# Performance work log

Hardware: AMD Instinct MI355X
Metric: run time of the kernel (lower is better)

The kernel has to match this reference:

```python
import jax, jax.numpy as jnp
import numpy as np

B, F, L, P, H = 32, 64, 8192, 96, 8
HD = F // H
EPS_ATTN = 1e-6
EPS_REVIN = 1e-5
EPS_LN = 1e-5


def setup_inputs() -> dict:
    key = jax.random.key(0)
    ks = jax.random.split(key, 8)
    f32 = jnp.float32
    return {
        'x': jax.random.normal(ks[0], (B, F, L), dtype=f32),
        'gamma': jnp.ones((1, 1, F), dtype=f32),
        'beta': jnp.zeros((1, 1, F), dtype=f32),
        'ln_w': jnp.ones((F,), dtype=f32),
        'ln_b': jnp.zeros((F,), dtype=f32),
        'Wq': 0.05 * jax.random.normal(ks[1], (F, F), dtype=f32),
        'bq': jnp.zeros((F,), dtype=f32),
        'Wk': 0.05 * jax.random.normal(ks[2], (F, F), dtype=f32),
        'bk': jnp.zeros((F,), dtype=f32),
        'Wv': 0.05 * jax.random.normal(ks[3], (F, F), dtype=f32),
        'bv': jnp.zeros((F,), dtype=f32),
        'Wo': 0.05 * jax.random.normal(ks[4], (F, F), dtype=f32),
        'bo': jnp.zeros((F,), dtype=f32),
        'Wlin': 0.01 * jax.random.normal(ks[5], (P, L), dtype=f32),
        'blin': jnp.zeros((P,), dtype=f32),
        'Wp': 0.1 * jax.random.normal(ks[6], (1, F), dtype=f32),
        'bp': jnp.zeros((1,), dtype=f32),
    }


def _phi(t):
    # feature map: elu(x) + 1 (non-negative)
    return jax.nn.elu(t) + 1.0


def _layernorm(h, w, b):
    mu = jnp.mean(h, axis=-1, keepdims=True)
    var = jnp.mean(jnp.square(h - mu), axis=-1, keepdims=True)
    return (h - mu) * jax.lax.rsqrt(var + EPS_LN) * w + b


def reference(x, gamma, beta, ln_w, ln_b, Wq, bq, Wk, bk, Wv, bv, Wo, bo,
              Wlin, blin, Wp, bp):
    # (B, F, L) -> (B, L, F)
    xt = jnp.transpose(x, (0, 2, 1))
    # RevIN norm (stats over time axis, detached; torch std is unbiased ddof=1)
    mean = jax.lax.stop_gradient(jnp.mean(xt, axis=1, keepdims=True))
    std = jax.lax.stop_gradient(jnp.std(xt, axis=1, keepdims=True, ddof=1) + EPS_REVIN)
    xn = (xt - mean) / std * gamma + beta
    residual = xn
    h = _layernorm(xn, ln_w, ln_b)
    # Q/K/V projections (torch Linear: h @ W.T + b)
    Q = h @ Wq.T + bq
    K = h @ Wk.T + bk
    V = h @ Wv.T + bv
    # (B, L, F) -> (B, H, L, HD)
    def heads(t):
        return jnp.transpose(t.reshape(B, L, H, HD), (0, 2, 1, 3))
    Q, K, V = heads(Q), heads(K), heads(V)
    Q, K = _phi(Q), _phi(K)
    # linear attention: phi(Q) (phi(K)^T V) / (phi(Q) sum_n phi(K))
    KV = jnp.einsum('bhnd,bhne->bhde', K, V)           # (B,H,HD,HD)
    out = jnp.einsum('bhnd,bhde->bhne', Q, KV)          # (B,H,L,HD)
    Z = jnp.sum(K, axis=2)                              # (B,H,HD)
    normalizer = jnp.einsum('bhnd,bhd->bhn', Q, Z)[..., None] + EPS_ATTN
    out = out / normalizer
    out = jnp.transpose(out, (0, 2, 1, 3)).reshape(B, L, F)
    out = out @ Wo.T + bo
    y = out + residual                                  # (B, L, F)
    # temporal linear: (B, F, L) @ Wlin.T -> (B, F, P) -> (B, P, F)
    y = jnp.transpose(jnp.transpose(y, (0, 2, 1)) @ Wlin.T + blin, (0, 2, 1))
    # RevIN denorm
    y = (y - beta) / gamma
    y = y * std + mean
    # projector to scalar per step
    return (y @ Wp.T + bp)[..., 0]                      # (B, P)
```

## Files before the change

kernel.cpp:

```cpp
#include <hip/hip_runtime.h>
#include <cstddef>

#define NB 32
#define NF 64
#define NL 8192
#define NP 96
#define NH 8
#define TSPLIT 32

#define WS_MEAN 0
#define WS_STD  2048
#define WS_RSTD 4096
#define WS_KV   6144
#define WS_Z    22528
#define WS_OUT2 24576
#define WS_MUN  221184
#define WS_RSN  483328
#define WS_WLB  745472
#define WS_XNB  1138688
#define WS_YT   9527296

typedef __bf16 bfx8 __attribute__((ext_vector_type(8)));
typedef float f32x4 __attribute__((ext_vector_type(4)));
#define MFMA16(a, b, c) __builtin_amdgcn_mfma_f32_16x16x32_bf16((a), (b), (c), 0, 0, 0)

__device__ __forceinline__ unsigned short f2bf(float f) {
  unsigned u = __float_as_uint(f);
  unsigned r = u + 0x7FFFu + ((u >> 16) & 1u);
  return (unsigned short)(r >> 16);
}
__device__ __forceinline__ unsigned packbf2(float lo, float hi) {
  return (unsigned)f2bf(lo) | ((unsigned)f2bf(hi) << 16);
}
__device__ __forceinline__ float bflo(unsigned d) { return __uint_as_float(d << 16); }
__device__ __forceinline__ float bfhi(unsigned d) { return __uint_as_float(d & 0xFFFF0000u); }
__device__ __forceinline__ float bf1(unsigned short s) { return __uint_as_float(((unsigned)s) << 16); }

__device__ __forceinline__ bfx8 ldfrag(const unsigned short* p) {
  uint4 u = *(const uint4*)p;
  return __builtin_bit_cast(bfx8, u);
}

__global__ __launch_bounds__(256) void k_pre(
    const float* __restrict__ x, const float* __restrict__ Wlin,
    float* __restrict__ wmean, float* __restrict__ wstd, float* __restrict__ wrstd,
    unsigned short* __restrict__ wlb, float* __restrict__ zz) {
  __shared__ float r1[4], r2[4];
  const int bid = blockIdx.x, tid = threadIdx.x;
  if (bid < NB * NF) {
    const float4* row4 = (const float4*)(x + (size_t)bid * NL);
    float s1 = 0.f, s2 = 0.f;
#pragma unroll
    for (int i = 0; i < NL / 4 / 256; i++) {
      float4 v = row4[tid + i * 256];
      s1 += v.x + v.y + v.z + v.w;
      s2 += v.x * v.x + v.y * v.y + v.z * v.z + v.w * v.w;
    }
#pragma unroll
    for (int off = 32; off > 0; off >>= 1) {
      s1 += __shfl_down(s1, off, 64);
      s2 += __shfl_down(s2, off, 64);
    }
    if ((tid & 63) == 0) { r1[tid >> 6] = s1; r2[tid >> 6] = s2; }
    __syncthreads();
    if (tid == 0) {
      s1 = r1[0] + r1[1] + r1[2] + r1[3];
      s2 = r2[0] + r2[1] + r2[2] + r2[3];
      float m = s1 * (1.f / NL);
      float var = (s2 - (float)NL * m * m) * (1.f / (NL - 1));
      float sd = sqrtf(fmaxf(var, 0.f)) + 1e-5f;
      wmean[bid] = m;
      wstd[bid] = sd;
      wrstd[bid] = 1.f / sd;
    }
    unsigned zi = (unsigned)bid * 256u + (unsigned)tid;
    if (zi < 215040u) zz[zi] = 0.f;
  } else {
    int i = (bid - NB * NF) * 256 + tid;
    int p = i >> 10;
    int l8 = (i & 1023) * 8;
    float4 va = *(const float4*)&Wlin[(size_t)p * NL + l8];
    float4 vb = *(const float4*)&Wlin[(size_t)p * NL + l8 + 4];
    uint4 o;
    o.x = packbf2(va.x, va.y); o.y = packbf2(va.z, va.w);
    o.z = packbf2(vb.x, vb.y); o.w = packbf2(vb.z, vb.w);
    *(uint4*)&wlb[(((size_t)(l8 >> 5)) * NP + p) * 32 + (l8 & 31)] = o;
  }
}

__global__ __launch_bounds__(256, 4) void k_kv(
    const float* __restrict__ x,
    const float* __restrict__ gamma, const float* __restrict__ beta,
    const float* __restrict__ lnw, const float* __restrict__ lnb,
    const float* __restrict__ Wk, const float* __restrict__ bk,
    const float* __restrict__ Wv, const float* __restrict__ bv,
    const float* __restrict__ wmean, const float* __restrict__ wrstd,
    float* __restrict__ wKV, float* __restrict__ wZ,
    float* __restrict__ wmun, float* __restrict__ wrsn,
    unsigned short* __restrict__ xnb) {
  __shared__ __align__(16) char smem[39936];
  unsigned short* hA  = (unsigned short*)smem;
  unsigned short* WkB = (unsigned short*)(smem + 18432);
  unsigned short* WvB = (unsigned short*)(smem + 27648);
  unsigned short* pK  = (unsigned short*)smem;
  unsigned short* pV  = (unsigned short*)(smem + 17408);
  float* SkT  = (float*)(smem + 36864);
  float* Tful = (float*)(smem + 37888);
  float* mun  = (float*)(smem + 38400);
  float* rsn  = (float*)(smem + 38912);
  float* cbc  = (float*)(smem + 39424);

  const int tid = threadIdx.x;
  const int b = blockIdx.x >> 6;
  const int tI = blockIdx.x & 63;
  const int L0 = tI * 128;
  const int lane = tid & 63, wv = tid >> 6;
  const int mm = lane & 15, qd = lane >> 4;

  if (tid < 64) {
    float cb = wrstd[b * NF + tid] * gamma[tid];
    cbc[2 * tid] = cb;
    cbc[2 * tid + 1] = beta[tid] - wmean[b * NF + tid] * cb;
  }
  {
    int jj = tid >> 2, g = tid & 3;
    int f0 = g * 16;
    float tkp = 0.f, tvp = 0.f;
#pragma unroll
    for (int i = 0; i < 4; i++) {
      int f = f0 + i * 4;
      float4 wk4 = *(const float4*)&Wk[jj * NF + f];
      float4 wv4 = *(const float4*)&Wv[jj * NF + f];
      float4 lw  = *(const float4*)&lnw[f];
      float4 lb  = *(const float4*)&lnb[f];
      uint2 pk2, pv2;
      pk2.x = packbf2(wk4.x * lw.x, wk4.y * lw.y);
      pk2.y = packbf2(wk4.z * lw.z, wk4.w * lw.w);
      pv2.x = packbf2(wv4.x * lw.x, wv4.y * lw.y);
      pv2.y = packbf2(wv4.z * lw.z, wv4.w * lw.w);
      *(uint2*)&WkB[jj * 72 + f] = pk2;
      *(uint2*)&WvB[jj * 72 + f] = pv2;
      tkp += lb.x * wk4.x + lb.y * wk4.y + lb.z * wk4.z + lb.w * wk4.w;
      tvp += lb.x * wv4.x + lb.y * wv4.y + lb.z * wv4.z + lb.w * wv4.w;
    }
    tkp += __shfl_xor(tkp, 1, 64); tkp += __shfl_xor(tkp, 2, 64);
    tvp += __shfl_xor(tvp, 1, 64); tvp += __shfl_xor(tvp, 2, 64);
    if (g == 0) { Tful[jj] = tkp; Tful[64 + jj] = tvp; }
  }
  __syncthreads();

  {
    const int l = tid >> 1, fh = tid & 1;
    const float* xp = x + ((size_t)(b * NF + fh * 32)) * NL + L0 + l;
    const float4* cb4 = (const float4*)&cbc[fh * 64];
    float s1 = 0.f, s2 = 0.f;
    unsigned pw[16];
#pragma unroll
    for (int f2 = 0; f2 < 16; f2++) {
      float4 c = cb4[f2];
      float v0 = xp[(size_t)(2 * f2) * NL];
      float v1 = xp[(size_t)(2 * f2 + 1) * NL];
      float a0 = fmaf(v0, c.x, c.y);
      float a1 = fmaf(v1, c.z, c.w);
      s1 += a0 + a1;
      s2 += fmaf(a0, a0, a1 * a1);
      pw[f2] = packbf2(a0, a1);
    }
    uint4 q[4];
#pragma unroll
    for (int i = 0; i < 4; i++) {
      q[i].x = pw[4 * i]; q[i].y = pw[4 * i + 1];
      q[i].z = pw[4 * i + 2]; q[i].w = pw[4 * i + 3];
    }
    uint4* hd = (uint4*)&hA[l * 72 + fh * 32];
    uint4* gd = (uint4*)(xnb + (((size_t)(b * 64 + tI) * 128 + l) * 64 + fh * 32));
#pragma unroll
    for (int i = 0; i < 4; i++) { hd[i] = q[i]; gd[i] = q[i]; }
    s1 += __shfl_xor(s1, 1, 64);
    s2 += __shfl_xor(s2, 1, 64);
    if (fh == 0) {
      float mu = s1 * (1.f / NF);
      float var = s2 * (1.f / NF) - mu * mu;
      float rs = rsqrtf(fmaxf(var, 0.f) + 1e-5f);
      mun[l] = mu; rsn[l] = rs;
      wmun[(size_t)b * NL + L0 + l] = mu;
      wrsn[(size_t)b * NL + L0 + l] = rs;
    }
  }
  if (tid >= 128) {
    int sel = (tid >> 6) - 2, j = tid & 63;
    const unsigned* wr = (const unsigned*)((sel ? WvB : WkB) + j * 72);
    float s = 0.f;
#pragma unroll
    for (int i = 0; i < 32; i++) { unsigned d = wr[i]; s += bflo(d) + bfhi(d); }
    float t = Tful[sel * 64 + j] + (sel ? bv[j] : bk[j]);
    SkT[sel * 128 + j] = s;
    SkT[sel * 128 + 64 + j] = t;
  }
  __syncthreads();

  const f32x4 fz = {0.f, 0.f, 0.f, 0.f};
  f32x4 kacc[2][4], vacc[2][4];
#pragma unroll
  for (int i = 0; i < 2; i++)
#pragma unroll
    for (int jt = 0; jt < 4; jt++) { kacc[i][jt] = fz; vacc[i][jt] = fz; }

#pragma unroll
  for (int kc = 0; kc < 2; kc++) {
    bfx8 a0 = ldfrag(&hA[(wv * 32 + mm) * 72 + kc * 32 + qd * 8]);
    bfx8 a1 = ldfrag(&hA[(wv * 32 + 16 + mm) * 72 + kc * 32 + qd * 8]);
#pragma unroll
    for (int jt = 0; jt < 4; jt++) {
      bfx8 bkf = ldfrag(&WkB[(jt * 16 + mm) * 72 + kc * 32 + qd * 8]);
      bfx8 bvf = ldfrag(&WvB[(jt * 16 + mm) * 72 + kc * 32 + qd * 8]);
      kacc[0][jt] = MFMA16(a0, bkf, kacc[0][jt]);
      kacc[1][jt] = MFMA16(a1, bkf, kacc[1][jt]);
      vacc[0][jt] = MFMA16(a0, bvf, vacc[0][jt]);
      vacc[1][jt] = MFMA16(a1, bvf, vacc[1][jt]);
    }
  }

#pragma unroll
  for (int lt2 = 0; lt2 < 2; lt2++) {
    float4 mu4 = *(const float4*)&mun[wv * 32 + lt2 * 16 + qd * 4];
    float4 rs4 = *(const float4*)&rsn[wv * 32 + lt2 * 16 + qd * 4];
    float muv[4] = {mu4.x, mu4.y, mu4.z, mu4.w};
    float rsv[4] = {rs4.x, rs4.y, rs4.z, rs4.w};
#pragma unroll
    for (int jt = 0; jt < 4; jt++) {
      int j = jt * 16 + mm;
      float Sk = SkT[j], Tk = SkT[64 + j], Sv = SkT[128 + j], Tv = SkT[192 + j];
#pragma unroll
      for (int r = 0; r < 4; r++) {
        float kk = rsv[r] * (kacc[lt2][jt][r] - muv[r] * Sk) + Tk;
        kacc[lt2][jt][r] = (kk > 0.f) ? (kk + 1.f) : __expf(kk);
        vacc[lt2][jt][r] = rsv[r] * (vacc[lt2][jt][r] - muv[r] * Sv) + Tv;
      }
    }
  }
  __syncthreads();

#pragma unroll
  for (int lt2 = 0; lt2 < 2; lt2++) {
    int l0 = wv * 32 + lt2 * 16 + qd * 4;
#pragma unroll
    for (int jt = 0; jt < 4; jt++) {
      int j = jt * 16 + mm;
      uint2 dk, dv;
      dk.x = packbf2(kacc[lt2][jt][0], kacc[lt2][jt][1]);
      dk.y = packbf2(kacc[lt2][jt][2], kacc[lt2][jt][3]);
      dv.x = packbf2(vacc[lt2][jt][0], vacc[lt2][jt][1]);
      dv.y = packbf2(vacc[lt2][jt][2], vacc[lt2][jt][3]);
      *(uint2*)&pK[j * 136 + l0] = dk;
      *(uint2*)&pV[j * 136 + l0] = dv;
    }
  }
  __syncthreads();

  {
    f32x4 racc = fz;
#pragma unroll
    for (int kb = 0; kb < 4; kb++) {
      bfx8 ak = ldfrag(&pK[(wv * 16 + mm) * 136 + kb * 32 + qd * 8]);
      bfx8 bv8 = ldfrag(&pV[(wv * 16 + mm) * 136 + kb * 32 + qd * 8]);
      racc = MFMA16(ak, bv8, racc);
    }
    int eh = mm >> 3, e = mm & 7;
#pragma unroll
    for (int r = 0; r < 4; r++) {
      int row = qd * 4 + r;
      if ((row >> 3) == eh)
        atomicAdd(&wKV[(b * NH + wv * 2 + eh) * 64 + (row & 7) * 8 + e], racc[r]);
    }
  }
  if (tid < 64) {
    const unsigned* kr = (const unsigned*)&pK[tid * 136];
    float zs = 0.f;
#pragma unroll
    for (int i = 0; i < 64; i++) { unsigned d = kr[i]; zs += bflo(d) + bfhi(d); }
    atomicAdd(&wZ[b * 64 + tid], zs);
  }
}

__global__ __launch_bounds__(256, 3) void k_qy(
    const unsigned short* __restrict__ xnb,
    const float* __restrict__ lnw, const float* __restrict__ lnb,
    const float* __restrict__ Wq, const float* __restrict__ bq,
    const float* __restrict__ Wo, const float* __restrict__ bo,
    const float* __restrict__ wmun, const float* __restrict__ wrsn,
    const float* __restrict__ wKV, const float* __restrict__ wZ,
    unsigned short* __restrict__ ytb) {
  __shared__ __align__(16) char smem[41728];
  unsigned short* hA  = (unsigned short*)smem;
  unsigned short* qaA = (unsigned short*)smem;
  unsigned short* WqB = (unsigned short*)(smem + 18432);
  unsigned short* WoB = (unsigned short*)(smem + 27648);
  float* kvz   = (float*)(smem + 36864);
  float* mun   = (float*)(smem + 39168);
  float* rsn   = (float*)(smem + 39680);
  float* SqTq  = (float*)(smem + 40192);
  float* Tpart = (float*)(smem + 40704);

  const int tid = threadIdx.x;
  const int b = blockIdx.x >> 6;
  const int tI = blockIdx.x & 63;
  const int L0 = tI * 128;
  const int lane = tid & 63, wv = tid >> 6;
  const int mm = lane & 15, qd = lane >> 4;
  const unsigned short* xtile = xnb + (size_t)(b * 64 + tI) * 128 * 64;

  {
    int jj = tid >> 2, g = tid & 3;
    int f0 = g * 16;
    float tqp = 0.f;
#pragma unroll
    for (int i = 0; i < 4; i++) {
      int f = f0 + i * 4;
      float4 wq4 = *(const float4*)&Wq[jj * NF + f];
      float4 wo4 = *(const float4*)&Wo[jj * NF + f];
      float4 lw  = *(const float4*)&lnw[f];
      float4 lb  = *(const float4*)&lnb[f];
      uint2 pq2, po2;
      pq2.x = packbf2(wq4.x * lw.x, wq4.y * lw.y);
      pq2.y = packbf2(wq4.z * lw.z, wq4.w * lw.w);
      po2.x = packbf2(wo4.x, wo4.y);
      po2.y = packbf2(wo4.z, wo4.w);
      *(uint2*)&WqB[jj * 72 + f] = pq2;
      *(uint2*)&WoB[jj * 72 + f] = po2;
      tqp += lb.x * wq4.x + lb.y * wq4.y + lb.z * wq4.z + lb.w * wq4.w;
    }
    Tpart[g * 64 + jj] = tqp;
  }
  for (int i = tid; i < 576; i += 256)
    kvz[i] = (i < 512) ? wKV[b * 512 + i] : wZ[b * 64 + i - 512];
  {
    int row = tid >> 1, half = tid & 1;
    const uint4* s4 = (const uint4*)(xtile + (size_t)row * 64 + half * 32);
    uint4 u0 = s4[0], u1 = s4[1], u2 = s4[2], u3 = s4[3];
    uint4* d4 = (uint4*)&hA[row * 72 + half * 32];
    d4[0] = u0; d4[1] = u1; d4[2] = u2; d4[3] = u3;
  }
  if (tid < 128) {
    mun[tid] = wmun[(size_t)b * NL + L0 + tid];
    rsn[tid] = wrsn[(size_t)b * NL + L0 + tid];
  }
  __syncthreads();

  if (tid < 64) {
    const unsigned* wr = (const unsigned*)(WqB + tid * 72);
    float s = 0.f;
#pragma unroll
    for (int i = 0; i < 32; i++) { unsigned d = wr[i]; s += bflo(d) + bfhi(d); }
    float t = Tpart[tid] + Tpart[64 + tid] + Tpart[128 + tid] + Tpart[192 + tid] + bq[tid];
    SqTq[tid] = s; SqTq[64 + tid] = t;
  }
  __syncthreads();

  const f32x4 fz = {0.f, 0.f, 0.f, 0.f};

  {
    f32x4 qacc[2][4];
#pragma unroll
    for (int i = 0; i < 2; i++)
#pragma unroll
      for (int jt = 0; jt < 4; jt++) qacc[i][jt] = fz;
#pragma unroll
    for (int kc = 0; kc < 2; kc++) {
      bfx8 a0 = ldfrag(&hA[(wv * 32 + mm) * 72 + kc * 32 + qd * 8]);
      bfx8 a1 = ldfrag(&hA[(wv * 32 + 16 + mm) * 72 + kc * 32 + qd * 8]);
#pragma unroll
      for (int jt = 0; jt < 4; jt++) {
        bfx8 bqf = ldfrag(&WqB[(jt * 16 + mm) * 72 + kc * 32 + qd * 8]);
        qacc[0][jt] = MFMA16(a0, bqf, qacc[0][jt]);
        qacc[1][jt] = MFMA16(a1, bqf, qacc[1][jt]);
      }
    }
#pragma unroll
    for (int lt2 = 0; lt2 < 2; lt2++) {
      float4 mu4 = *(const float4*)&mun[wv * 32 + lt2 * 16 + qd * 4];
      float4 rs4 = *(const float4*)&rsn[wv * 32 + lt2 * 16 + qd * 4];
      float muv[4] = {mu4.x, mu4.y, mu4.z, mu4.w};
      float rsv[4] = {rs4.x, rs4.y, rs4.z, rs4.w};
      int l0 = wv * 32 + lt2 * 16 + qd * 4;
#pragma unroll
      for (int jt = 0; jt < 4; jt++) {
        int j = jt * 16 + mm;
        float Sj = SqTq[j], Tj = SqTq[64 + j];
#pragma unroll
        for (int r = 0; r < 4; r++) {
          float q = rsv[r] * (qacc[lt2][jt][r] - muv[r] * Sj) + Tj;
          q = (q > 0.f) ? (q + 1.f) : __expf(q);
          qaA[(l0 + r) * 72 + j] = f2bf(q);
        }
      }
    }
  }
  __syncthreads();

  {
    int lt = tid & 31, hd = tid >> 5;
    int lbase = lt * 4;
    float qv[4][8];
#pragma unroll
    for (int i = 0; i < 4; i++) {
      uint4 u = *(const uint4*)&qaA[(lbase + i) * 72 + hd * 8];
      qv[i][0] = bflo(u.x); qv[i][1] = bfhi(u.x);
      qv[i][2] = bflo(u.y); qv[i][3] = bfhi(u.y);
      qv[i][4] = bflo(u.z); qv[i][5] = bfhi(u.z);
      qv[i][6] = bflo(u.w); qv[i][7] = bfhi(u.w);
    }
    float att[4][8], nrm[4];
#pragma unroll
    for (int i = 0; i < 4; i++) {
      nrm[i] = 1e-6f;
#pragma unroll
      for (int e = 0; e < 8; e++) att[i][e] = 0.f;
    }
#pragma unroll
    for (int d = 0; d < 8; d++) {
      float zd = kvz[512 + hd * 8 + d];
      float4 kva = *(const float4*)&kvz[hd * 64 + d * 8];
      float4 kvb = *(const float4*)&kvz[hd * 64 + d * 8 + 4];
#pragma unroll
      for (int i = 0; i < 4; i++) {
        float qq = qv[i][d];
        nrm[i] = fmaf(qq, zd, nrm[i]);
        att[i][0] = fmaf(qq, kva.x, att[i][0]);
        att[i][1] = fmaf(qq, kva.y, att[i][1]);
        att[i][2] = fmaf(qq, kva.z, att[i][2]);
        att[i][3] = fmaf(qq, kva.w, att[i][3]);
        att[i][4] = fmaf(qq, kvb.x, att[i][4]);
        att[i][5] = fmaf(qq, kvb.y, att[i][5]);
        att[i][6] = fmaf(qq, kvb.z, att[i][6]);
        att[i][7] = fmaf(qq, kvb.w, att[i][7]);
      }
    }
#pragma unroll
    for (int i = 0; i < 4; i++) {
      float inv = 1.f / nrm[i];
      uint4 o;
      o.x = packbf2(att[i][0] * inv, att[i][1] * inv);
      o.y = packbf2(att[i][2] * inv, att[i][3] * inv);
      o.z = packbf2(att[i][4] * inv, att[i][5] * inv);
      o.w = packbf2(att[i][6] * inv, att[i][7] * inv);
      *(uint4*)&qaA[(lbase + i) * 72 + hd * 8] = o;
    }
  }
  __syncthreads();

  {
    f32x4 yacc[2][4];
#pragma unroll
    for (int i = 0; i < 2; i++)
#pragma unroll
      for (int ft = 0; ft < 4; ft++) yacc[i][ft] = fz;
#pragma unroll
    for (int ec = 0; ec < 2; ec++) {
      bfx8 a0 = ldfrag(&qaA[(wv * 32 + mm) * 72 + ec * 32 + qd * 8]);
      bfx8 a1 = ldfrag(&qaA[(wv * 32 + 16 + mm) * 72 + ec * 32 + qd * 8]);
#pragma unroll
      for (int ft = 0; ft < 4; ft++) {
        bfx8 bof = ldfrag(&WoB[(ft * 16 + mm) * 72 + ec * 32 + qd * 8]);
        yacc[0][ft] = MFMA16(a0, bof, yacc[0][ft]);
        yacc[1][ft] = MFMA16(a1, bof, yacc[1][ft]);
      }
    }
#pragma unroll
    for (int lt2 = 0; lt2 < 2; lt2++) {
      int l0 = wv * 32 + lt2 * 16 + qd * 4;
#pragma unroll
      for (int ft = 0; ft < 4; ft++) {
        int ff = ft * 16 + mm;
        float bof = bo[ff];
        float v0 = yacc[lt2][ft][0] + bf1(xtile[(size_t)(l0 + 0) * 64 + ff]) + bof;
        float v1 = yacc[lt2][ft][1] + bf1(xtile[(size_t)(l0 + 1) * 64 + ff]) + bof;
        float v2 = yacc[lt2][ft][2] + bf1(xtile[(size_t)(l0 + 2) * 64 + ff]) + bof;
        float v3 = yacc[lt2][ft][3] + bf1(xtile[(size_t)(l0 + 3) * 64 + ff]) + bof;
        uint2 o2;
        o2.x = packbf2(v0, v1);
        o2.y = packbf2(v2, v3);
        size_t idx = (((size_t)b * (NL / 32) + (L0 >> 5) + wv) * 64 + ff) * 32 + lt2 * 16 + qd * 4;
        *(uint2*)&ytb[idx] = o2;
      }
    }
  }
}

__global__ __launch_bounds__(256) void k_temporal(
    const unsigned short* __restrict__ ytb, const unsigned short* __restrict__ wlb,
    float* __restrict__ out2) {
  const int tid = threadIdx.x, lane = tid & 63, wvx = tid >> 6;
  const int mm = lane & 15, qd = lane >> 4;
  const int b = blockIdx.x / TSPLIT;
  const int kc = blockIdx.x % TSPLIT;
  const f32x4 fz = {0.f, 0.f, 0.f, 0.f};
  f32x4 acc[6];
#pragma unroll
  for (int pt = 0; pt < 6; pt++) acc[pt] = fz;

#pragma unroll 2
  for (int ks = 0; ks < 8; ks++) {
    int lg = kc * 8 + ks;
    bfx8 bfr = ldfrag(&ytb[(((size_t)b * (NL / 32) + lg) * 64 + wvx * 16 + mm) * 32 + qd * 8]);
#pragma unroll
    for (int pt = 0; pt < 6; pt++) {
      bfx8 afr = ldfrag(&wlb[((size_t)lg * NP + pt * 16 + mm) * 32 + qd * 8]);
      acc[pt] = MFMA16(afr, bfr, acc[pt]);
    }
  }
  const int ff = wvx * 16 + mm;
#pragma unroll
  for (int pt = 0; pt < 6; pt++) {
#pragma unroll
    for (int r = 0; r < 4; r++) {
      int p = pt * 16 + qd * 4 + r;
      atomicAdd(&out2[((size_t)(b * NP + p)) * NF + ff], acc[pt][r]);
    }
  }
}

__global__ __launch_bounds__(64) void k_final(
    const float* __restrict__ out2, const float* __restrict__ blin,
    const float* __restrict__ gamma, const float* __restrict__ beta,
    const float* __restrict__ wmean, const float* __restrict__ wstd,
    const float* __restrict__ Wp, const float* __restrict__ bp,
    float* __restrict__ out) {
  int b = blockIdx.x / NP;
  int p = blockIdx.x % NP;
  int f = threadIdx.x;
  float v = out2[((size_t)(b * NP + p)) * NF + f] + blin[p];
  v = (v - beta[f]) / gamma[f];
  v = v * wstd[b * NF + f] + wmean[b * NF + f];
  float s = v * Wp[f];
#pragma unroll
  for (int off = 32; off > 0; off >>= 1)
    s += __shfl_down(s, off, 64);
  if (f == 0) out[blockIdx.x] = s + bp[0];
}

extern "C" void kernel_launch(void* const* d_in, const int* in_sizes, int n_in,
                              void* d_out, int out_size, void* d_ws, size_t ws_size,
                              hipStream_t stream) {
  const float* x     = (const float*)d_in[0];
  const float* gamma = (const float*)d_in[1];
  const float* beta  = (const float*)d_in[2];
  const float* lnw   = (const float*)d_in[3];
  const float* lnb   = (const float*)d_in[4];
  const float* Wq    = (const float*)d_in[5];
  const float* bq    = (const float*)d_in[6];
  const float* Wk    = (const float*)d_in[7];
  const float* bk    = (const float*)d_in[8];
  const float* Wv    = (const float*)d_in[9];
  const float* bv    = (const float*)d_in[10];
  const float* Wo    = (const float*)d_in[11];
  const float* bo    = (const float*)d_in[12];
  const float* Wlin  = (const float*)d_in[13];
  const float* blin  = (const float*)d_in[14];
  const float* Wp    = (const float*)d_in[15];
  const float* bp    = (const float*)d_in[16];
  float* out = (float*)d_out;
  float* ws  = (float*)d_ws;

  float* wmean = ws + WS_MEAN;
  float* wstd  = ws + WS_STD;
  float* wrstd = ws + WS_RSTD;
  float* wKV   = ws + WS_KV;
  float* wZ    = ws + WS_Z;
  float* wout2 = ws + WS_OUT2;
  float* wmun  = ws + WS_MUN;
  float* wrsn  = ws + WS_RSN;
  unsigned short* wlb = (unsigned short*)(ws + WS_WLB);
  unsigned short* xnb = (unsigned short*)(ws + WS_XNB);
  unsigned short* ytb = (unsigned short*)(ws + WS_YT);

  k_pre<<<NB * NF + NP * NL / 8 / 256, 256, 0, stream>>>(x, Wlin, wmean, wstd, wrstd, wlb, wKV);
  k_kv<<<NB * 64, 256, 0, stream>>>(x, gamma, beta, lnw, lnb, Wk, bk, Wv, bv,
                                    wmean, wrstd, wKV, wZ, wmun, wrsn, xnb);
  k_qy<<<NB * 64, 256, 0, stream>>>(xnb, lnw, lnb, Wq, bq, Wo, bo,
                                    wmun, wrsn, wKV, wZ, ytb);
  k_temporal<<<NB * TSPLIT, 256, 0, stream>>>(ytb, wlb, wout2);
  k_final<<<NB * NP, 64, 0, stream>>>(wout2, blin, gamma, beta, wmean, wstd, Wp, bp, out);
}
```

Measured before the change: 227.6 us.

## Vectorize x loads, fold weight-sum reductions into staging, preload residual from LDS

In k_kv each thread now loads float4 vectors covering four timesteps and eight features, in place of scalar strided loads, and reduces the LayerNorm statistics with cross-lane shuffles. The per-row weight sums (Sk/Sv/Sq) are computed while the weights are converted to bf16, which removes a serial LDS pass and one barrier in k_qy. The Z sum is taken from register accumulators before the bf16 round-trip, and k_qy seeds its output accumulator with the residual read from LDS plus bo instead of re-reading xtile from global memory. Trimmed shared memory lets k_qy's launch bound rise to 4 blocks, though the extra live yacc registers across the Q phase could add register pressure.

```diff
diff --git a/kernel.cpp b/kernel.cpp
--- a/kernel.cpp
+++ b/kernel.cpp
@@ -98,17 +98,16 @@
     float* __restrict__ wKV, float* __restrict__ wZ,
     float* __restrict__ wmun, float* __restrict__ wrsn,
     unsigned short* __restrict__ xnb) {
-  __shared__ __align__(16) char smem[39936];
+  __shared__ __align__(16) char smem[39424];
   unsigned short* hA  = (unsigned short*)smem;
   unsigned short* WkB = (unsigned short*)(smem + 18432);
   unsigned short* WvB = (unsigned short*)(smem + 27648);
   unsigned short* pK  = (unsigned short*)smem;
   unsigned short* pV  = (unsigned short*)(smem + 17408);
   float* SkT  = (float*)(smem + 36864);
-  float* Tful = (float*)(smem + 37888);
-  float* mun  = (float*)(smem + 38400);
-  float* rsn  = (float*)(smem + 38912);
-  float* cbc  = (float*)(smem + 39424);
+  float* mun  = (float*)(smem + 37888);
+  float* rsn  = (float*)(smem + 38400);
+  float* cbc  = (float*)(smem + 38912);
 
   const int tid = threadIdx.x;
   const int b = blockIdx.x >> 6;
@@ -125,7 +124,7 @@
   {
     int jj = tid >> 2, g = tid & 3;
     int f0 = g * 16;
-    float tkp = 0.f, tvp = 0.f;
+    float tkp = 0.f, tvp = 0.f, skp = 0.f, svp = 0.f;
 #pragma unroll
     for (int i = 0; i < 4; i++) {
       int f = f0 + i * 4;
@@ -142,60 +141,84 @@
       *(uint2*)&WvB[jj * 72 + f] = pv2;
       tkp += lb.x * wk4.x + lb.y * wk4.y + lb.z * wk4.z + lb.w * wk4.w;
       tvp += lb.x * wv4.x + lb.y * wv4.y + lb.z * wv4.z + lb.w * wv4.w;
+      skp += bflo(pk2.x) + bfhi(pk2.x) + bflo(pk2.y) + bfhi(pk2.y);
+      svp += bflo(pv2.x) + bfhi(pv2.x) + bflo(pv2.y) + bfhi(pv2.y);
     }
     tkp += __shfl_xor(tkp, 1, 64); tkp += __shfl_xor(tkp, 2, 64);
     tvp += __shfl_xor(tvp, 1, 64); tvp += __shfl_xor(tvp, 2, 64);
-    if (g == 0) { Tful[jj] = tkp; Tful[64 + jj] = tvp; }
+    skp += __shfl_xor(skp, 1, 64); skp += __shfl_xor(skp, 2, 64);
+    svp += __shfl_xor(svp, 1, 64); svp += __shfl_xor(svp, 2, 64);
+    if (g == 0) {
+      SkT[jj]       = skp;
+      SkT[64 + jj]  = tkp + bk[jj];
+      SkT[128 + jj] = svp;
+      SkT[192 + jj] = tvp + bv[jj];
+    }
   }
   __syncthreads();
 
   {
-    const int l = tid >> 1, fh = tid & 1;
-    const float* xp = x + ((size_t)(b * NF + fh * 32)) * NL + L0 + l;
-    const float4* cb4 = (const float4*)&cbc[fh * 64];
-    float s1 = 0.f, s2 = 0.f;
-    unsigned pw[16];
-#pragma unroll
-    for (int f2 = 0; f2 < 16; f2++) {
-      float4 c = cb4[f2];
-      float v0 = xp[(size_t)(2 * f2) * NL];
-      float v1 = xp[(size_t)(2 * f2 + 1) * NL];
-      float a0 = fmaf(v0, c.x, c.y);
-      float a1 = fmaf(v1, c.z, c.w);
-      s1 += a0 + a1;
-      s2 += fmaf(a0, a0, a1 * a1);
-      pw[f2] = packbf2(a0, a1);
-    }
-    uint4 q[4];
+    const int lt = tid >> 3;
+    const int fg = tid & 7;
+    const int l0q = lt * 4;
+    const float* xp = x + ((size_t)(b * NF + fg * 8)) * NL + L0 + l0q;
+    f32x4 v[8];
+#pragma unroll
+    for (int i = 0; i < 8; i++) v[i] = *(const f32x4*)(xp + (size_t)i * NL);
+    float a[8][4];
 #pragma unroll
     for (int i = 0; i < 4; i++) {
-      q[i].x = pw[4 * i]; q[i].y = pw[4 * i + 1];
-      q[i].z = pw[4 * i + 2]; q[i].w = pw[4 * i + 3];
-    }
-    uint4* hd = (uint4*)&hA[l * 72 + fh * 32];
-    uint4* gd = (uint4*)(xnb + (((size_t)(b * 64 + tI) * 128 + l) * 64 + fh * 32));
-#pragma unroll
-    for (int i = 0; i < 4; i++) { hd[i] = q[i]; gd[i] = q[i]; }
-    s1 += __shfl_xor(s1, 1, 64);
-    s2 += __shfl_xor(s2, 1, 64);
-    if (fh == 0) {
-      float mu = s1 * (1.f / NF);
-      float var = s2 * (1.f / NF) - mu * mu;
-      float rs = rsqrtf(fmaxf(var, 0.f) + 1e-5f);
-      mun[l] = mu; rsn[l] = rs;
-      wmun[(size_t)b * NL + L0 + l] = mu;
-      wrsn[(size_t)b * NL + L0 + l] = rs;
-    }
-  }
-  if (tid >= 128) {
-    int sel = (tid >> 6) - 2, j = tid & 63;
-    const unsigned* wr = (const unsigned*)((sel ? WvB : WkB) + j * 72);
-    float s = 0.f;
-#pragma unroll
-    for (int i = 0; i < 32; i++) { unsigned d = wr[i]; s += bflo(d) + bfhi(d); }
-    float t = Tful[sel * 64 + j] + (sel ? bv[j] : bk[j]);
-    SkT[sel * 128 + j] = s;
-    SkT[sel * 128 + 64 + j] = t;
+      float4 c = *(const float4*)&cbc[fg * 16 + i * 4];
+#pragma unroll
+      for (int j = 0; j < 4; j++) {
+        a[2 * i][j]     = fmaf(v[2 * i][j], c.x, c.y);
+        a[2 * i + 1][j] = fmaf(v[2 * i + 1][j], c.z, c.w);
+      }
+    }
+    float s1[4], s2[4];
+#pragma unroll
+    for (int j = 0; j < 4; j++) {
+      s1[j] = 0.f; s2[j] = 0.f;
+#pragma unroll
+      for (int i = 0; i < 8; i++) {
+        s1[j] += a[i][j];
+        s2[j] = fmaf(a[i][j], a[i][j], s2[j]);
+      }
+    }
+#pragma unroll
+    for (int m = 1; m <= 4; m <<= 1) {
+#pragma unroll
+      for (int j = 0; j < 4; j++) {
+        s1[j] += __shfl_xor(s1[j], m, 64);
+        s2[j] += __shfl_xor(s2[j], m, 64);
+      }
+    }
+#pragma unroll
+    for (int j = 0; j < 4; j++) {
+      uint4 o;
+      o.x = packbf2(a[0][j], a[1][j]);
+      o.y = packbf2(a[2][j], a[3][j]);
+      o.z = packbf2(a[4][j], a[5][j]);
+      o.w = packbf2(a[6][j], a[7][j]);
+      *(uint4*)&hA[(l0q + j) * 72 + fg * 8] = o;
+      *(uint4*)(xnb + (((size_t)(b * 64 + tI) * 128 + l0q + j) * 64 + fg * 8)) = o;
+    }
+    if (fg == 0) {
+      float mv[4], rv[4];
+#pragma unroll
+      for (int j = 0; j < 4; j++) {
+        float mu = s1[j] * (1.f / NF);
+        float var = s2[j] * (1.f / NF) - mu * mu;
+        mv[j] = mu;
+        rv[j] = rsqrtf(fmaxf(var, 0.f) + 1e-5f);
+      }
+      float4 m4 = {mv[0], mv[1], mv[2], mv[3]};
+      float4 r4 = {rv[0], rv[1], rv[2], rv[3]};
+      *(float4*)&mun[l0q] = m4;
+      *(float4*)&rsn[l0q] = r4;
+      *(float4*)&wmun[(size_t)b * NL + L0 + l0q] = m4;
+      *(float4*)&wrsn[(size_t)b * NL + L0 + l0q] = r4;
+    }
   }
   __syncthreads();
 
@@ -237,6 +260,20 @@
         kacc[lt2][jt][r] = (kk > 0.f) ? (kk + 1.f) : __expf(kk);
         vacc[lt2][jt][r] = rsv[r] * (vacc[lt2][jt][r] - muv[r] * Sv) + Tv;
       }
+    }
+  }
+
+  {
+#pragma unroll
+    for (int jt = 0; jt < 4; jt++) {
+      float z = 0.f;
+#pragma unroll
+      for (int lt2 = 0; lt2 < 2; lt2++)
+#pragma unroll
+        for (int r = 0; r < 4; r++) z += kacc[lt2][jt][r];
+      z += __shfl_xor(z, 16, 64);
+      z += __shfl_xor(z, 32, 64);
+      if (qd == 0) atomicAdd(&wZ[b * 64 + jt * 16 + mm], z);
     }
   }
   __syncthreads();
@@ -274,16 +311,9 @@
         atomicAdd(&wKV[(b * NH + wv * 2 + eh) * 64 + (row & 7) * 8 + e], racc[r]);
     }
   }
-  if (tid < 64) {
-    const unsigned* kr = (const unsigned*)&pK[tid * 136];
-    float zs = 0.f;
-#pragma unroll
-    for (int i = 0; i < 64; i++) { unsigned d = kr[i]; zs += bflo(d) + bfhi(d); }
-    atomicAdd(&wZ[b * 64 + tid], zs);
-  }
-}
-
-__global__ __launch_bounds__(256, 3) void k_qy(
+}
+
+__global__ __launch_bounds__(256, 4) void k_qy(
     const unsigned short* __restrict__ xnb,
     const float* __restrict__ lnw, const float* __restrict__ lnb,
     const float* __restrict__ Wq, const float* __restrict__ bq,
@@ -291,16 +321,15 @@
     const float* __restrict__ wmun, const float* __restrict__ wrsn,
     const float* __restrict__ wKV, const float* __restrict__ wZ,
     unsigned short* __restrict__ ytb) {
-  __shared__ __align__(16) char smem[41728];
+  __shared__ __align__(16) char smem[40960];
   unsigned short* hA  = (unsigned short*)smem;
   unsigned short* qaA = (unsigned short*)smem;
   unsigned short* WqB = (unsigned short*)(smem + 18432);
   unsigned short* WoB = (unsigned short*)(smem + 27648);
   float* kvz   = (float*)(smem + 36864);
-  float* mun   = (float*)(smem + 39168);
-  float* rsn   = (float*)(smem + 39680);
-  float* SqTq  = (float*)(smem + 40192);
-  float* Tpart = (float*)(smem + 40704);
+  float* mun   = (float*)(smem + 39424);
+  float* rsn   = (float*)(smem + 39936);
+  float* SqTq  = (float*)(smem + 40448);
 
   const int tid = threadIdx.x;
   const int b = blockIdx.x >> 6;
@@ -313,7 +342,7 @@
   {
     int jj = tid >> 2, g = tid & 3;
     int f0 = g * 16;
-    float tqp = 0.f;
+    float tqp = 0.f, sqp = 0.f;
 #pragma unroll
     for (int i = 0; i < 4; i++) {
       int f = f0 + i * 4;
@@ -329,11 +358,14 @@
       *(uint2*)&WqB[jj * 72 + f] = pq2;
       *(uint2*)&WoB[jj * 72 + f] = po2;
       tqp += lb.x * wq4.x + lb.y * wq4.y + lb.z * wq4.z + lb.w * wq4.w;
-    }
-    Tpart[g * 64 + jj] = tqp;
-  }
-  for (int i = tid; i < 576; i += 256)
-    kvz[i] = (i < 512) ? wKV[b * 512 + i] : wZ[b * 64 + i - 512];
+      sqp += bflo(pq2.x) + bfhi(pq2.x) + bflo(pq2.y) + bfhi(pq2.y);
+    }
+    tqp += __shfl_xor(tqp, 1, 64); tqp += __shfl_xor(tqp, 2, 64);
+    sqp += __shfl_xor(sqp, 1, 64); sqp += __shfl_xor(sqp, 2, 64);
+    if (g == 0) { SqTq[jj] = sqp; SqTq[64 + jj] = tqp + bq[jj]; }
+  }
+  for (int i = tid; i < 640; i += 256)
+    kvz[i] = (i < 512) ? wKV[b * 512 + i] : (i < 576 ? wZ[b * 64 + i - 512] : bo[i - 576]);
   {
     int row = tid >> 1, half = tid & 1;
     const uint4* s4 = (const uint4*)(xtile + (size_t)row * 64 + half * 32);
@@ -341,23 +373,16 @@
     uint4* d4 = (uint4*)&hA[row * 72 + half * 32];
     d4[0] = u0; d4[1] = u1; d4[2] = u2; d4[3] = u3;
   }
-  if (tid < 128) {
-    mun[tid] = wmun[(size_t)b * NL + L0 + tid];
-    rsn[tid] = wrsn[(size_t)b * NL + L0 + tid];
+  if (tid < 64) {
+    int h = tid >> 5, i = tid & 31;
+    const float* src = h ? wrsn : wmun;
+    float4 v = *(const float4*)&src[(size_t)b * NL + L0 + i * 4];
+    *(float4*)&((h ? rsn : mun)[i * 4]) = v;
   }
   __syncthreads();
 
-  if (tid < 64) {
-    const unsigned* wr = (const unsigned*)(WqB + tid * 72);
-    float s = 0.f;
-#pragma unroll
-    for (int i = 0; i < 32; i++) { unsigned d = wr[i]; s += bflo(d) + bfhi(d); }
-    float t = Tpart[tid] + Tpart[64 + tid] + Tpart[128 + tid] + Tpart[192 + tid] + bq[tid];
-    SqTq[tid] = s; SqTq[64 + tid] = t;
-  }
-  __syncthreads();
-
   const f32x4 fz = {0.f, 0.f, 0.f, 0.f};
+  f32x4 yacc[2][4];
 
   {
     f32x4 qacc[2][4];
@@ -374,6 +399,18 @@
         bfx8 bqf = ldfrag(&WqB[(jt * 16 + mm) * 72 + kc * 32 + qd * 8]);
         qacc[0][jt] = MFMA16(a0, bqf, qacc[0][jt]);
         qacc[1][jt] = MFMA16(a1, bqf, qacc[1][jt]);
+      }
+    }
+#pragma unroll
+    for (int lt2 = 0; lt2 < 2; lt2++) {
+      int l0 = wv * 32 + lt2 * 16 + qd * 4;
+#pragma unroll
+      for (int ft = 0; ft < 4; ft++) {
+        int ff = ft * 16 + mm;
+        float bof = kvz[576 + ff];
+#pragma unroll
+        for (int r = 0; r < 4; r++)
+          yacc[lt2][ft][r] = bf1(hA[(l0 + r) * 72 + ff]) + bof;
       }
     }
 #pragma unroll
@@ -450,11 +487,6 @@
   __syncthreads();
 
   {
-    f32x4 yacc[2][4];
-#pragma unroll
-    for (int i = 0; i < 2; i++)
-#pragma unroll
-      for (int ft = 0; ft < 4; ft++) yacc[i][ft] = fz;
 #pragma unroll
     for (int ec = 0; ec < 2; ec++) {
       bfx8 a0 = ldfrag(&qaA[(wv * 32 + mm) * 72 + ec * 32 + qd * 8]);
@@ -468,18 +500,12 @@
     }
 #pragma unroll
     for (int lt2 = 0; lt2 < 2; lt2++) {
-      int l0 = wv * 32 + lt2 * 16 + qd * 4;
 #pragma unroll
       for (int ft = 0; ft < 4; ft++) {
         int ff = ft * 16 + mm;
-        float bof = bo[ff];
-        float v0 = yacc[lt2][ft][0] + bf1(xtile[(size_t)(l0 + 0) * 64 + ff]) + bof;
-        float v1 = yacc[lt2][ft][1] + bf1(xtile[(size_t)(l0 + 1) * 64 + ff]) + bof;
-        float v2 = yacc[lt2][ft][2] + bf1(xtile[(size_t)(l0 + 2) * 64 + ff]) + bof;
-        float v3 = yacc[lt2][ft][3] + bf1(xtile[(size_t)(l0 + 3) * 64 + ff]) + bof;
         uint2 o2;
-        o2.x = packbf2(v0, v1);
-        o2.y = packbf2(v2, v3);
+        o2.x = packbf2(yacc[lt2][ft][0], yacc[lt2][ft][1]);
+        o2.y = packbf2(yacc[lt2][ft][2], yacc[lt2][ft][3]);
         size_t idx = (((size_t)b * (NL / 32) + (L0 >> 5) + wv) * 64 + ff) * 32 + lt2 * 16 + qd * 4;
         *(uint2*)&ytb[idx] = o2;
       }
```

Result: no change. 230.5 us (+1.3%).
